# Kernel tuning notes

Measured on AMD Instinct MI355X. Metric: run time of the kernel, lower is better.

Reference implementation:

```python
import jax, jax.numpy as jnp
import numpy as np

N_NODES = 50000
N_EDGES = 800000
N_ENTS = 200000
N_RELS = 500
D = 128


def setup_inputs() -> dict:
    key = jax.random.key(0)
    ks = jax.random.split(key, 9)
    return {
        "prev_ent_embs": jax.random.normal(ks[0], (N_ENTS, D), dtype=jnp.float32),
        "rel_embs": jax.random.normal(ks[1], (N_RELS, D), dtype=jnp.float32),
        "loop_weight": jax.random.normal(ks[2], (D, D), dtype=jnp.float32) * 0.1,
        "evolve_loop_weight": jax.random.normal(ks[3], (D, D), dtype=jnp.float32) * 0.1,
        "weight_neighbor": jax.random.normal(ks[4], (D, D), dtype=jnp.float32) * 0.1,
        "node_id": jax.random.randint(ks[5], (N_NODES,), 0, N_ENTS, dtype=jnp.int64) if jax.config.jax_enable_x64 else jax.random.randint(ks[5], (N_NODES,), 0, N_ENTS, dtype=jnp.int32),
        "src": jax.random.randint(ks[6], (N_EDGES,), 0, N_NODES, dtype=jnp.int32),
        "dst": jax.random.randint(ks[7], (N_EDGES,), 0, N_NODES, dtype=jnp.int32),
        "etype": jax.random.randint(ks[8], (N_EDGES,), 0, N_RELS, dtype=jnp.int32),
    }


def reference(prev_ent_embs, rel_embs, loop_weight, evolve_loop_weight,
              weight_neighbor, node_id, src, dst, etype):
    n_nodes = node_id.shape[0]
    # node features gathered from global entity table
    h = prev_ent_embs[node_id]                                    # [N, D]

    # per-edge message: (h[src] + rel[type]) @ W_neighbor
    msg = (h[src] + rel_embs[etype]) @ weight_neighbor            # [E, D]

    # scatter-sum into destination nodes
    agg = jax.ops.segment_sum(msg, dst, num_segments=n_nodes)     # [N, D]

    # in-degree and norm (apply_func: h * in_norm, standard 1/in_degree)
    deg = jax.ops.segment_sum(jnp.ones_like(dst, dtype=h.dtype), dst,
                              num_segments=n_nodes)               # [N]
    has_in = deg > 0
    in_norm = jnp.where(has_in, 1.0 / jnp.maximum(deg, 1.0), 0.0)[:, None]
    agg = agg * in_norm

    # self-loop: loop_weight where in_degree>0, evolve_loop_weight otherwise
    loop_msg = jnp.where(has_in[:, None], h @ loop_weight, h @ evolve_loop_weight)

    # activation (dropout=0 -> identity in eval)
    return jax.nn.relu(agg + loop_msg)
```

## Files before the change

### kernel.cpp

```cpp
#include <hip/hip_runtime.h>
#include <hip/hip_bf16.h>
#include <stdint.h>

#define N_NODES 50000
#define N_EDGES 800000
#define N_ENTS  200000
#define N_RELS  500
#define DIM     128

using f32x4  = __attribute__((ext_vector_type(4))) float;
using bf16x8 = __attribute__((ext_vector_type(8))) short;

static __device__ __forceinline__ ushort f_to_bf16(float f) {
    __hip_bfloat16 h = __float2bfloat16(f);
    return *reinterpret_cast<ushort*>(&h);
}
static __device__ __forceinline__ uint pack2(float a, float b) {
    return (uint)f_to_bf16(a) | ((uint)f_to_bf16(b) << 16);
}
static __device__ __forceinline__ float blo(uint u) { return __uint_as_float(u << 16); }
static __device__ __forceinline__ float bhi(uint u) { return __uint_as_float(u & 0xffff0000u); }

__global__ __launch_bounds__(256) void k_front(
        const float* __restrict__ prev, const int* __restrict__ node_id,
        ushort* __restrict__ afull,
        const int* __restrict__ dst, int* __restrict__ deg,
        const float* __restrict__ rel, ushort* __restrict__ rel_bf,
        const float* __restrict__ Wn, const float* __restrict__ Wl,
        ushort* __restrict__ WfT) {
    int blk = blockIdx.x;
    if (blk < 3125) {
        int e = blk * 256 + threadIdx.x;
        if (e < N_EDGES) atomicAdd(&deg[dst[e]], 1);
    } else if (blk < 6250) {
        int i = (blk - 3125) * 256 + threadIdx.x;
        int row = i >> 4, c = (i & 15) * 8;
        int nid = node_id[row];
        const float* p = prev + (size_t)nid * DIM + c;
        float4 v0 = *(const float4*)p;
        float4 v1 = *(const float4*)(p + 4);
        uint4 w;
        w.x = pack2(v0.x, v0.y);
        w.y = pack2(v0.z, v0.w);
        w.z = pack2(v1.x, v1.y);
        w.w = pack2(v1.z, v1.w);
        *(uint4*)(afull + (size_t)row * 256 + 128 + c) = w;
    } else {
        int i = (blk - 6250) * 256 + threadIdx.x;
        if (i < 128 * 256) {
            int n = i >> 8, k = i & 255;
            float v = (k < 128) ? Wn[k * 128 + n] : Wl[(k - 128) * 128 + n];
            WfT[i] = f_to_bf16(v);
        } else {
            int j = i - 128 * 256;
            if (j < N_RELS * 64) {
                float2 v = *(const float2*)(rel + j * 2);
                *(uint*)(rel_bf + j * 2) = pack2(v.x, v.y);
            }
        }
    }
}

__global__ __launch_bounds__(256) void k_offs(const int* __restrict__ deg,
                                              int* __restrict__ counter,
                                              int* __restrict__ offs,
                                              int* __restrict__ cursor) {
    int i = blockIdx.x * 256 + threadIdx.x;
    int lane = threadIdx.x & 63;
    int v = (i < N_NODES) ? deg[i] : 0;
    int inc = v;
#pragma unroll
    for (int o = 1; o < 64; o <<= 1) {
        int u = __shfl_up(inc, o);
        if (lane >= o) inc += u;
    }
    int wsum = __shfl(inc, 63);
    int base = 0;
    if (lane == 0) base = atomicAdd(counter, wsum);
    base = __shfl(base, 0);
    if (i < N_NODES) {
        int off = base + inc - v;
        offs[i]   = off;
        cursor[i] = off;
    }
}

__global__ __launch_bounds__(256) void k_fill(const int* __restrict__ dst,
                                              const int* __restrict__ src,
                                              const int* __restrict__ etype,
                                              int* __restrict__ cursor,
                                              uint* __restrict__ srcpk) {
    int e = blockIdx.x * blockDim.x + threadIdx.x;
    if (e < N_EDGES) {
        uint rec = (uint)src[e] | ((uint)etype[e] << 16);
        int p = atomicAdd(&cursor[dst[e]], 1);
        srcpk[p] = rec;
    }
}

__global__ __launch_bounds__(256) void k_agg(ushort* __restrict__ afull,
                                             const ushort* __restrict__ rel_bf,
                                             const uint* __restrict__ srcpk,
                                             const int* __restrict__ offs,
                                             const int* __restrict__ deg) {
    int wave = threadIdx.x >> 6, lane = threadIdx.x & 63;
    int n = blockIdx.x * 4 + wave;
    if (n >= N_NODES) return;
    int off = offs[n], d = deg[n];
    int c = lane * 2;
    const ushort* hb = afull + 128 + c;
    const ushort* rb = rel_bf + c;
    float a0 = 0.f, a1 = 0.f;
    for (int b0 = 0; b0 < d; b0 += 64) {
        int cnt = min(64, d - b0);
        int rec = (lane < cnt) ? (int)srcpk[off + b0 + lane] : 0;
        int j = 0;
        for (; j + 4 <= cnt; j += 4) {
            uint e0 = (uint)__shfl(rec, j);
            uint e1 = (uint)__shfl(rec, j + 1);
            uint e2 = (uint)__shfl(rec, j + 2);
            uint e3 = (uint)__shfl(rec, j + 3);
            uint h0 = *(const uint*)(hb + (size_t)(e0 & 0xffffu) * 256);
            uint r0 = *(const uint*)(rb + (e0 >> 16) * 128);
            uint h1 = *(const uint*)(hb + (size_t)(e1 & 0xffffu) * 256);
            uint r1 = *(const uint*)(rb + (e1 >> 16) * 128);
            uint h2 = *(const uint*)(hb + (size_t)(e2 & 0xffffu) * 256);
            uint r2 = *(const uint*)(rb + (e2 >> 16) * 128);
            uint h3 = *(const uint*)(hb + (size_t)(e3 & 0xffffu) * 256);
            uint r3 = *(const uint*)(rb + (e3 >> 16) * 128);
            a0 += blo(h0) + blo(r0); a1 += bhi(h0) + bhi(r0);
            a0 += blo(h1) + blo(r1); a1 += bhi(h1) + bhi(r1);
            a0 += blo(h2) + blo(r2); a1 += bhi(h2) + bhi(r2);
            a0 += blo(h3) + blo(r3); a1 += bhi(h3) + bhi(r3);
        }
        for (; j < cnt; j++) {
            uint e0 = (uint)__shfl(rec, j);
            uint h0 = *(const uint*)(hb + (size_t)(e0 & 0xffffu) * 256);
            uint r0 = *(const uint*)(rb + (e0 >> 16) * 128);
            a0 += blo(h0) + blo(r0); a1 += bhi(h0) + bhi(r0);
        }
    }
    float norm = (d > 0) ? 1.0f / (float)d : 0.0f;
    *(uint*)(afull + (size_t)n * 256 + c) = pack2(a0 * norm, a1 * norm);
}

#define LDSK 264
__global__ __launch_bounds__(256) void k_mm(const ushort* __restrict__ afull,
                                            const ushort* __restrict__ WfT,
                                            float* __restrict__ out) {
    __shared__ ushort wl[128 * LDSK];
    for (int idx = threadIdx.x; idx < 128 * 32; idx += 256) {
        int n = idx >> 5, p = idx & 31;
        uint4 v = *(const uint4*)(WfT + n * 256 + p * 8);
        *(uint4*)(&wl[n * LDSK + p * 8]) = v;
    }
    __syncthreads();

    int wave = threadIdx.x >> 6, lane = threadIdx.x & 63;
    int m = lane & 15, quad = lane >> 4;
    int rowBase = blockIdx.x * 128 + wave * 32;

    f32x4 acc[2][8];
#pragma unroll
    for (int rt = 0; rt < 2; rt++)
#pragma unroll
        for (int ct = 0; ct < 8; ct++) acc[rt][ct] = f32x4{0.f, 0.f, 0.f, 0.f};

    int r0 = rowBase + m;      if (r0 > N_NODES - 1) r0 = N_NODES - 1;
    int r1 = rowBase + 16 + m; if (r1 > N_NODES - 1) r1 = N_NODES - 1;
    const ushort* pa0 = afull + (size_t)r0 * 256 + quad * 8;
    const ushort* pa1 = afull + (size_t)r1 * 256 + quad * 8;

#pragma unroll
    for (int ks = 0; ks < 8; ks++) {
        bf16x8 a0 = *(const bf16x8*)(pa0 + ks * 32);
        bf16x8 a1 = *(const bf16x8*)(pa1 + ks * 32);
#pragma unroll
        for (int ct = 0; ct < 8; ct++) {
            bf16x8 b = *(const bf16x8*)(&wl[(ct * 16 + m) * LDSK + ks * 32 + quad * 8]);
            acc[0][ct] = __builtin_amdgcn_mfma_f32_16x16x32_bf16(a0, b, acc[0][ct], 0, 0, 0);
            acc[1][ct] = __builtin_amdgcn_mfma_f32_16x16x32_bf16(a1, b, acc[1][ct], 0, 0, 0);
        }
    }

#pragma unroll
    for (int rt = 0; rt < 2; rt++) {
        int rbase = rowBase + rt * 16 + quad * 4;
#pragma unroll
        for (int reg = 0; reg < 4; reg++) {
            int grow = rbase + reg;
            if (grow < N_NODES) {
#pragma unroll
                for (int ct = 0; ct < 8; ct++) {
                    float v = acc[rt][ct][reg];
                    out[(size_t)grow * 128 + ct * 16 + m] = v > 0.f ? v : 0.f;
                }
            }
        }
    }
}

__global__ void k_fixup(const ushort* __restrict__ afull,
                        const float* __restrict__ We,
                        const int* __restrict__ deg,
                        float* __restrict__ out) {
    int wave = threadIdx.x >> 6, lane = threadIdx.x & 63;
    int n = blockIdx.x * 4 + wave;
    if (n >= N_NODES) return;
    if (deg[n] != 0) return;
    int c = lane * 2;
    float a0 = 0.f, a1 = 0.f;
    for (int k = 0; k < 128; k++) {
        float h = blo((uint)afull[(size_t)n * 256 + 128 + k]);
        a0 += h * We[k * 128 + c];
        a1 += h * We[k * 128 + c + 1];
    }
    out[(size_t)n * 128 + c]     = a0 > 0.f ? a0 : 0.f;
    out[(size_t)n * 128 + c + 1] = a1 > 0.f ? a1 : 0.f;
}

extern "C" void kernel_launch(void* const* d_in, const int* in_sizes, int n_in,
                              void* d_out, int out_size, void* d_ws, size_t ws_size,
                              hipStream_t stream) {
    const float* prev  = (const float*)d_in[0];
    const float* rel   = (const float*)d_in[1];
    const float* Wl    = (const float*)d_in[2];
    const float* We    = (const float*)d_in[3];
    const float* Wn    = (const float*)d_in[4];
    const int* node_id = (const int*)d_in[5];
    const int* src     = (const int*)d_in[6];
    const int* dst     = (const int*)d_in[7];
    const int* etype   = (const int*)d_in[8];
    float* out = (float*)d_out;

    char* ws = (char*)d_ws;
    ushort* afull  = (ushort*)(ws);
    ushort* WfT    = (ushort*)(ws + 25600000);
    ushort* rel_bf = (ushort*)(ws + 25665536);
    int* deg       = (int*)(ws + 25793536);
    int* counter   = (int*)(ws + 25993536);
    int* offs      = (int*)(ws + 25993600);
    int* cursor    = (int*)(ws + 26193600);
    uint* srcpk    = (uint*)(ws + 26393600);

    hipMemsetAsync(deg, 0, 200064, stream);
    k_front <<<6504, 256, 0, stream>>>(prev, node_id, afull, dst, deg,
                                       rel, rel_bf, Wn, Wl, WfT);
    k_offs  <<<196,  256, 0, stream>>>(deg, counter, offs, cursor);
    k_fill  <<<3125, 256, 0, stream>>>(dst, src, etype, cursor, srcpk);
    k_agg   <<<12500, 256, 0, stream>>>(afull, rel_bf, srcpk, offs, deg);
    k_mm    <<<391,  256, 0, stream>>>(afull, WfT, out);
    k_fixup <<<12500, 256, 0, stream>>>(afull, We, deg, out);
}
```

Measured before the change: 300.6 us.

## Capture atomic rank during degree count to drop cursor atomics; pad degree counters

The degree-counting atomic now returns each edge's rank within its destination, stored as a 16-bit value, so the fill pass computes slot positions as offset plus rank with no second atomic pass or cursor array. Degree counters are spaced 16 ints apart (64 bytes) to reduce cache-line contention between neighbouring nodes. The gather loop in aggregation is unrolled from 4 to 8 edges to keep more loads in flight. The trade-off is a much larger memset, extra rank traffic, and scattered, uncoalesced reads of the padded degree array.

Result: faster. 265.2 us (-11.8%).

```diff
diff --git a/kernel.cpp b/kernel.cpp
--- a/kernel.cpp
+++ b/kernel.cpp
@@ -8,6 +8,8 @@
 #define N_RELS  500
 #define DIM     128
 
+#define DEGS 16
+
 using f32x4  = __attribute__((ext_vector_type(4))) float;
 using bf16x8 = __attribute__((ext_vector_type(8))) short;
 
@@ -25,13 +27,17 @@
         const float* __restrict__ prev, const int* __restrict__ node_id,
         ushort* __restrict__ afull,
         const int* __restrict__ dst, int* __restrict__ deg,
+        ushort* __restrict__ r16,
         const float* __restrict__ rel, ushort* __restrict__ rel_bf,
         const float* __restrict__ Wn, const float* __restrict__ Wl,
         ushort* __restrict__ WfT) {
     int blk = blockIdx.x;
     if (blk < 3125) {
         int e = blk * 256 + threadIdx.x;
-        if (e < N_EDGES) atomicAdd(&deg[dst[e]], 1);
+        if (e < N_EDGES) {
+            int r = atomicAdd(&deg[dst[e] * DEGS], 1);
+            r16[e] = (ushort)r;
+        }
     } else if (blk < 6250) {
         int i = (blk - 3125) * 256 + threadIdx.x;
         int row = i >> 4, c = (i & 15) * 8;
@@ -63,11 +69,10 @@
 
 __global__ __launch_bounds__(256) void k_offs(const int* __restrict__ deg,
                                               int* __restrict__ counter,
-                                              int* __restrict__ offs,
-                                              int* __restrict__ cursor) {
+                                              int* __restrict__ offs) {
     int i = blockIdx.x * 256 + threadIdx.x;
     int lane = threadIdx.x & 63;
-    int v = (i < N_NODES) ? deg[i] : 0;
+    int v = (i < N_NODES) ? deg[i * DEGS] : 0;
     int inc = v;
 #pragma unroll
     for (int o = 1; o < 64; o <<= 1) {
@@ -78,22 +83,19 @@
     int base = 0;
     if (lane == 0) base = atomicAdd(counter, wsum);
     base = __shfl(base, 0);
-    if (i < N_NODES) {
-        int off = base + inc - v;
-        offs[i]   = off;
-        cursor[i] = off;
-    }
-}
-
-__global__ __launch_bounds__(256) void k_fill(const int* __restrict__ dst,
-                                              const int* __restrict__ src,
-                                              const int* __restrict__ etype,
-                                              int* __restrict__ cursor,
-                                              uint* __restrict__ srcpk) {
+    if (i < N_NODES) offs[i] = base + inc - v;
+}
+
+__global__ __launch_bounds__(256) void k_scatter(const int* __restrict__ dst,
+                                                 const int* __restrict__ src,
+                                                 const int* __restrict__ etype,
+                                                 const ushort* __restrict__ r16,
+                                                 const int* __restrict__ offs,
+                                                 uint* __restrict__ srcpk) {
     int e = blockIdx.x * blockDim.x + threadIdx.x;
     if (e < N_EDGES) {
         uint rec = (uint)src[e] | ((uint)etype[e] << 16);
-        int p = atomicAdd(&cursor[dst[e]], 1);
+        int p = offs[dst[e]] + (int)r16[e];
         srcpk[p] = rec;
     }
 }
@@ -106,7 +108,7 @@
     int wave = threadIdx.x >> 6, lane = threadIdx.x & 63;
     int n = blockIdx.x * 4 + wave;
     if (n >= N_NODES) return;
-    int off = offs[n], d = deg[n];
+    int off = offs[n], d = deg[n * DEGS];
     int c = lane * 2;
     const ushort* hb = afull + 128 + c;
     const ushort* rb = rel_bf + c;
@@ -115,23 +117,43 @@
         int cnt = min(64, d - b0);
         int rec = (lane < cnt) ? (int)srcpk[off + b0 + lane] : 0;
         int j = 0;
-        for (; j + 4 <= cnt; j += 4) {
-            uint e0 = (uint)__shfl(rec, j);
-            uint e1 = (uint)__shfl(rec, j + 1);
-            uint e2 = (uint)__shfl(rec, j + 2);
-            uint e3 = (uint)__shfl(rec, j + 3);
-            uint h0 = *(const uint*)(hb + (size_t)(e0 & 0xffffu) * 256);
-            uint r0 = *(const uint*)(rb + (e0 >> 16) * 128);
-            uint h1 = *(const uint*)(hb + (size_t)(e1 & 0xffffu) * 256);
-            uint r1 = *(const uint*)(rb + (e1 >> 16) * 128);
-            uint h2 = *(const uint*)(hb + (size_t)(e2 & 0xffffu) * 256);
-            uint r2 = *(const uint*)(rb + (e2 >> 16) * 128);
-            uint h3 = *(const uint*)(hb + (size_t)(e3 & 0xffffu) * 256);
-            uint r3 = *(const uint*)(rb + (e3 >> 16) * 128);
+        for (; j + 8 <= cnt; j += 8) {
+            uint h0, h1, h2, h3, h4, h5, h6, h7;
+            uint r0, r1, r2, r3, r4, r5, r6, r7;
+            {
+                uint e0 = (uint)__shfl(rec, j);
+                uint e1 = (uint)__shfl(rec, j + 1);
+                uint e2 = (uint)__shfl(rec, j + 2);
+                uint e3 = (uint)__shfl(rec, j + 3);
+                uint e4 = (uint)__shfl(rec, j + 4);
+                uint e5 = (uint)__shfl(rec, j + 5);
+                uint e6 = (uint)__shfl(rec, j + 6);
+                uint e7 = (uint)__shfl(rec, j + 7);
+                h0 = *(const uint*)(hb + (size_t)(e0 & 0xffffu) * 256);
+                r0 = *(const uint*)(rb + (e0 >> 16) * 128);
+                h1 = *(const uint*)(hb + (size_t)(e1 & 0xffffu) * 256);
+                r1 = *(const uint*)(rb + (e1 >> 16) * 128);
+                h2 = *(const uint*)(hb + (size_t)(e2 & 0xffffu) * 256);
+                r2 = *(const uint*)(rb + (e2 >> 16) * 128);
+                h3 = *(const uint*)(hb + (size_t)(e3 & 0xffffu) * 256);
+                r3 = *(const uint*)(rb + (e3 >> 16) * 128);
+                h4 = *(const uint*)(hb + (size_t)(e4 & 0xffffu) * 256);
+                r4 = *(const uint*)(rb + (e4 >> 16) * 128);
+                h5 = *(const uint*)(hb + (size_t)(e5 & 0xffffu) * 256);
+                r5 = *(const uint*)(rb + (e5 >> 16) * 128);
+                h6 = *(const uint*)(hb + (size_t)(e6 & 0xffffu) * 256);
+                r6 = *(const uint*)(rb + (e6 >> 16) * 128);
+                h7 = *(const uint*)(hb + (size_t)(e7 & 0xffffu) * 256);
+                r7 = *(const uint*)(rb + (e7 >> 16) * 128);
+            }
             a0 += blo(h0) + blo(r0); a1 += bhi(h0) + bhi(r0);
             a0 += blo(h1) + blo(r1); a1 += bhi(h1) + bhi(r1);
             a0 += blo(h2) + blo(r2); a1 += bhi(h2) + bhi(r2);
             a0 += blo(h3) + blo(r3); a1 += bhi(h3) + bhi(r3);
+            a0 += blo(h4) + blo(r4); a1 += bhi(h4) + bhi(r4);
+            a0 += blo(h5) + blo(r5); a1 += bhi(h5) + bhi(r5);
+            a0 += blo(h6) + blo(r6); a1 += bhi(h6) + bhi(r6);
+            a0 += blo(h7) + blo(r7); a1 += bhi(h7) + bhi(r7);
         }
         for (; j < cnt; j++) {
             uint e0 = (uint)__shfl(rec, j);
@@ -207,7 +229,7 @@
     int wave = threadIdx.x >> 6, lane = threadIdx.x & 63;
     int n = blockIdx.x * 4 + wave;
     if (n >= N_NODES) return;
-    if (deg[n] != 0) return;
+    if (deg[n * DEGS] != 0) return;
     int c = lane * 2;
     float a0 = 0.f, a1 = 0.f;
     for (int k = 0; k < 128; k++) {
@@ -238,17 +260,17 @@
     ushort* WfT    = (ushort*)(ws + 25600000);
     ushort* rel_bf = (ushort*)(ws + 25665536);
     int* deg       = (int*)(ws + 25793536);
-    int* counter   = (int*)(ws + 25993536);
-    int* offs      = (int*)(ws + 25993600);
-    int* cursor    = (int*)(ws + 26193600);
-    uint* srcpk    = (uint*)(ws + 26393600);
-
-    hipMemsetAsync(deg, 0, 200064, stream);
-    k_front <<<6504, 256, 0, stream>>>(prev, node_id, afull, dst, deg,
-                                       rel, rel_bf, Wn, Wl, WfT);
-    k_offs  <<<196,  256, 0, stream>>>(deg, counter, offs, cursor);
-    k_fill  <<<3125, 256, 0, stream>>>(dst, src, etype, cursor, srcpk);
-    k_agg   <<<12500, 256, 0, stream>>>(afull, rel_bf, srcpk, offs, deg);
-    k_mm    <<<391,  256, 0, stream>>>(afull, WfT, out);
-    k_fixup <<<12500, 256, 0, stream>>>(afull, We, deg, out);
-}
+    int* counter   = (int*)(ws + 28993536);
+    int* offs      = (int*)(ws + 28993600);
+    ushort* r16    = (ushort*)(ws + 29193600);
+    uint* srcpk    = (uint*)(ws + 30793600);
+
+    hipMemsetAsync(deg, 0, 3200064, stream);
+    k_front   <<<6504, 256, 0, stream>>>(prev, node_id, afull, dst, deg, r16,
+                                         rel, rel_bf, Wn, Wl, WfT);
+    k_offs    <<<196,  256, 0, stream>>>(deg, counter, offs);
+    k_scatter <<<3125, 256, 0, stream>>>(dst, src, etype, r16, offs, srcpk);
+    k_agg     <<<12500, 256, 0, stream>>>(afull, rel_bf, srcpk, offs, deg);
+    k_mm      <<<391,  256, 0, stream>>>(afull, WfT, out);
+    k_fixup   <<<12500, 256, 0, stream>>>(afull, We, deg, out);
+}
```
